# Optimization experiments

Measured on AMD Instinct MI355X. Metric: run time of the kernel, lower is better.

The kernel has to match this reference:

```python
import jax, jax.numpy as jnp
import numpy as np

ALPHA = 0.05
GDEP = 3
HID = 20  # self.hidden_num in the torch module


def setup_inputs() -> dict:
    key = jax.random.key(0)
    ks = jax.random.split(key, 6)
    B, C_IN, N, C = 8, 32, 1024, 16
    C_OUT = 32
    x = jax.random.normal(ks[0], (B, C_IN, N, C), dtype=jnp.float32)
    adj = jax.random.uniform(ks[1], (B, C, N, N), dtype=jnp.float32)
    W_start = jax.random.normal(ks[2], (C_IN, HID), dtype=jnp.float32) / np.sqrt(C_IN)
    b_start = jax.random.normal(ks[3], (HID,), dtype=jnp.float32) * 0.01
    W_end = jax.random.normal(ks[4], (HID * (GDEP + 1), C_OUT), dtype=jnp.float32) / np.sqrt(HID * (GDEP + 1))
    b_end = jax.random.normal(ks[5], (C_OUT,), dtype=jnp.float32) * 0.01
    return {"x": x, "adj": adj, "W_start": W_start, "b_start": b_start,
            "W_end": W_end, "b_end": b_end}


def reference(x, adj, W_start, b_start, W_end, b_end):
    # x: [B, c_in, N, C]; adj: [B, C, N, N]
    N = adj.shape[-1]
    # vectorized degree normalization: A_hat = (A + I) / rowsum(A + I)
    A = adj + jnp.eye(N, dtype=adj.dtype)
    A = A / A.sum(axis=-1, keepdims=True)
    # transpose(1,3) then mlp_start -> h0: [B, C, N, HID]
    xt = jnp.transpose(x, (0, 3, 2, 1))
    h0 = jnp.einsum('bcni,ih->bcnh', xt, W_start) + b_start
    h = h0
    outs = [h0]
    for _ in range(GDEP):
        # torch einsum 'ncwl,ncvw->ncvl' == A[b,c,v,w] @ h[b,c,w,l]
        h = ALPHA * h0 + (1.0 - ALPHA) * jnp.einsum('bcvw,bcwh->bcvh', A, h)
        outs.append(h)
    ho = jnp.concatenate(outs, axis=-1)  # [B, C, N, HID*(GDEP+1)]
    return jnp.einsum('bcnk,ko->bcno', ho, W_end) + b_end
```

## Files before the change

### kernel.cpp

```cpp
#include <hip/hip_runtime.h>
#include <hip/hip_bf16.h>
#include <stdint.h>

#define ALPHA 0.05f
constexpr int B_   = 8;
constexpr int CIN  = 32;
constexpr int NN   = 1024;
constexpr int CC   = 16;
constexpr int HID_ = 20;
constexpr int COUT = 32;
constexpr int PAIRS = B_ * CC;

typedef __attribute__((ext_vector_type(8))) short bf8;
typedef __attribute__((ext_vector_type(4))) float f4;

__device__ inline unsigned short f2bf(float x) {
    union { float f; uint32_t u; } v; v.f = x;
    uint32_t u = v.u;
    u += 0x7fffu + ((u >> 16) & 1u);
    return (unsigned short)(u >> 16);
}

__device__ inline bf8 pack8(float4 lo, float4 hi) {
    bf8 r;
    r[0] = (short)f2bf(lo.x); r[1] = (short)f2bf(lo.y);
    r[2] = (short)f2bf(lo.z); r[3] = (short)f2bf(lo.w);
    r[4] = (short)f2bf(hi.x); r[5] = (short)f2bf(hi.y);
    r[6] = (short)f2bf(hi.z); r[7] = (short)f2bf(hi.w);
    return r;
}

__global__ __launch_bounds__(256) void k_h0(const float* __restrict__ x,
                                            const float* __restrict__ Ws,
                                            const float* __restrict__ bs,
                                            float* __restrict__ h0) {
    int b = blockIdx.y, n0 = blockIdx.x * 16;
    __shared__ float xs[CIN * 16 * CC];
    __shared__ float WsS[CIN * HID_];
    __shared__ float bsS[HID_];
    int t = threadIdx.x;

    #pragma unroll
    for (int j = 0; j < 8; j++) {
        int idx = t + j * 256;
        int i = idx >> 6, f = idx & 63;
        ((float4*)xs)[idx] =
            ((const float4*)(x + ((size_t)(b * CIN + i) * NN + n0) * CC))[f];
    }
    for (int j = t; j < CIN * HID_; j += 256) WsS[j] = Ws[j];
    if (t < HID_) bsS[t] = bs[t];
    __syncthreads();

    int c = t & 15, nl = t >> 4;
    float acc[HID_];
    #pragma unroll
    for (int l = 0; l < HID_; l++) acc[l] = bsS[l];
    for (int i = 0; i < CIN; i++) {
        float xv = xs[i * 256 + nl * 16 + c];
        #pragma unroll
        for (int l = 0; l < HID_; l++) acc[l] += xv * WsS[i * HID_ + l];
    }
    float* dst = h0 + ((size_t)(b * CC + c) * NN + (n0 + nl)) * HID_;
    #pragma unroll
    for (int l = 0; l < HID_; l++) dst[l] = acc[l];
}

constexpr int BSTR = 1032;

__global__ __launch_bounds__(512, 4) void k_prop(
        const float* __restrict__ adj,
        const float* __restrict__ h_in,
        const float* __restrict__ h0,
        float* __restrict__ h_out) {
    int pair = blockIdx.y;
    int m0 = blockIdx.x * 256;
    __shared__ unsigned short Ht[32 * BSTR];
    int t = threadIdx.x;
    int lane = t & 63, wave = t >> 6;
    int ml = lane & 15, quad = lane >> 4;

    const float* hp = h_in + (size_t)pair * NN * HID_;
    for (int k = t; k < NN; k += 512) {
        float4 v0 = *(const float4*)(hp + (size_t)k * HID_ + 0);
        float4 v1 = *(const float4*)(hp + (size_t)k * HID_ + 4);
        float4 v2 = *(const float4*)(hp + (size_t)k * HID_ + 8);
        float4 v3 = *(const float4*)(hp + (size_t)k * HID_ + 12);
        float4 v4 = *(const float4*)(hp + (size_t)k * HID_ + 16);
        float vv[20] = {v0.x, v0.y, v0.z, v0.w, v1.x, v1.y, v1.z, v1.w,
                        v2.x, v2.y, v2.z, v2.w, v3.x, v3.y, v3.z, v3.w,
                        v4.x, v4.y, v4.z, v4.w};
        #pragma unroll
        for (int l = 0; l < HID_; l++) Ht[l * BSTR + k] = f2bf(vv[l]);
    }
    {
        uint4 ones; ones.x = ones.y = ones.z = ones.w = 0x3F803F80u;
        uint4 zero; zero.x = zero.y = zero.z = zero.w = 0u;
        for (int idx = t; idx < 12 * (NN / 8); idx += 512) {
            int row = 20 + (idx >> 7), seg = idx & 127;
            *(uint4*)&Ht[row * BSTR + seg * 8] = (row == 20) ? ones : zero;
        }
    }
    __syncthreads();

    f4 acc[2][2];
    #pragma unroll
    for (int mt = 0; mt < 2; mt++)
        #pragma unroll
        for (int nt = 0; nt < 2; nt++)
            #pragma unroll
            for (int r = 0; r < 4; r++) acc[mt][nt][r] = 0.0f;

    const float* a0p = adj + ((size_t)pair * NN + (m0 + wave * 32 + ml)) * NN + quad * 8;
    const float* a1p = a0p + (size_t)16 * NN;
    const int b0off = ml * BSTR + quad * 8;
    const int b1off = b0off + 16 * BSTR;

    float4 c00 = *(const float4*)(a0p + 0);
    float4 c01 = *(const float4*)(a0p + 4);
    float4 c10 = *(const float4*)(a1p + 0);
    float4 c11 = *(const float4*)(a1p + 4);

    #pragma unroll 1
    for (int ks = 0; ks < NN; ks += 64) {
        float4 n00 = *(const float4*)(a0p + ks + 32);
        float4 n01 = *(const float4*)(a0p + ks + 36);
        float4 n10 = *(const float4*)(a1p + ks + 32);
        float4 n11 = *(const float4*)(a1p + ks + 36);
        {
            bf8 b0 = *(const bf8*)&Ht[b0off + ks];
            bf8 b1 = *(const bf8*)&Ht[b1off + ks];
            bf8 a0 = pack8(c00, c01);
            bf8 a1 = pack8(c10, c11);
            acc[0][0] = __builtin_amdgcn_mfma_f32_16x16x32_bf16(a0, b0, acc[0][0], 0, 0, 0);
            acc[0][1] = __builtin_amdgcn_mfma_f32_16x16x32_bf16(a0, b1, acc[0][1], 0, 0, 0);
            acc[1][0] = __builtin_amdgcn_mfma_f32_16x16x32_bf16(a1, b0, acc[1][0], 0, 0, 0);
            acc[1][1] = __builtin_amdgcn_mfma_f32_16x16x32_bf16(a1, b1, acc[1][1], 0, 0, 0);
        }
        int k2 = (ks + 64 < NN) ? (ks + 64) : 0;
        c00 = *(const float4*)(a0p + k2);
        c01 = *(const float4*)(a0p + k2 + 4);
        c10 = *(const float4*)(a1p + k2);
        c11 = *(const float4*)(a1p + k2 + 4);
        {
            bf8 b0 = *(const bf8*)&Ht[b0off + ks + 32];
            bf8 b1 = *(const bf8*)&Ht[b1off + ks + 32];
            bf8 a0 = pack8(n00, n01);
            bf8 a1 = pack8(n10, n11);
            acc[0][0] = __builtin_amdgcn_mfma_f32_16x16x32_bf16(a0, b0, acc[0][0], 0, 0, 0);
            acc[0][1] = __builtin_amdgcn_mfma_f32_16x16x32_bf16(a0, b1, acc[0][1], 0, 0, 0);
            acc[1][0] = __builtin_amdgcn_mfma_f32_16x16x32_bf16(a1, b0, acc[1][0], 0, 0, 0);
            acc[1][1] = __builtin_amdgcn_mfma_f32_16x16x32_bf16(a1, b1, acc[1][1], 0, 0, 0);
        }
    }

    #pragma unroll
    for (int mt = 0; mt < 2; mt++) {
        #pragma unroll
        for (int r = 0; r < 4; r++) {
            int row = m0 + wave * 32 + mt * 16 + quad * 4 + r;
            float s = __shfl(acc[mt][1][r], (quad << 4) + 4, 64) + 1.0f;
            float inv_s = (1.0f - ALPHA) / s;
            {
                size_t off = ((size_t)pair * NN + row) * HID_ + ml;
                h_out[off] = ALPHA * h0[off] + inv_s * (acc[mt][0][r] + h_in[off]);
            }
            if (ml < 4) {
                size_t off = ((size_t)pair * NN + row) * HID_ + 16 + ml;
                h_out[off] = ALPHA * h0[off] + inv_s * (acc[mt][1][r] + h_in[off]);
            }
        }
    }
}

__global__ __launch_bounds__(256) void k_out(const float* __restrict__ h0,
                                             const float* __restrict__ h1,
                                             const float* __restrict__ h2,
                                             const float* __restrict__ h3,
                                             const float* __restrict__ We,
                                             const float* __restrict__ be,
                                             float* __restrict__ out) {
    int pair = blockIdx.y, n0 = blockIdx.x * 128;
    int t = threadIdx.x;
    __shared__ float WeT[32 * 84];
    __shared__ float beS[32];
    for (int idx = t; idx < 80 * 32; idx += 256) {
        int k = idx >> 5, o = idx & 31;
        WeT[o * 84 + k] = We[idx];
    }
    if (t < 32) beS[t] = be[t];
    __syncthreads();

    const float* hs[4] = {h0, h1, h2, h3};
    int og = t & 7, ng = t >> 3;
    float acc[4][4];
    #pragma unroll
    for (int r = 0; r < 4; r++)
        #pragma unroll
        for (int c = 0; c < 4; c++) acc[r][c] = beS[og + c * 8];

    #pragma unroll
    for (int src = 0; src < 4; src++) {
        const float* hp = hs[src] + ((size_t)pair * NN + n0 + ng) * HID_;
        #pragma unroll
        for (int j = 0; j < 5; j++) {
            float4 hv[4];
            #pragma unroll
            for (int r = 0; r < 4; r++)
                hv[r] = *(const float4*)(hp + (size_t)(r * 32) * HID_ + j * 4);
            #pragma unroll
            for (int c = 0; c < 4; c++) {
                float4 wv = *(const float4*)&WeT[(og + c * 8) * 84 + src * 20 + j * 4];
                #pragma unroll
                for (int r = 0; r < 4; r++)
                    acc[r][c] += hv[r].x * wv.x + hv[r].y * wv.y +
                                 hv[r].z * wv.z + hv[r].w * wv.w;
            }
        }
    }
    #pragma unroll
    for (int r = 0; r < 4; r++)
        #pragma unroll
        for (int c = 0; c < 4; c++)
            out[((size_t)pair * NN + n0 + ng + r * 32) * COUT + og + c * 8] = acc[r][c];
}

extern "C" void kernel_launch(void* const* d_in, const int* in_sizes, int n_in,
                              void* d_out, int out_size, void* d_ws, size_t ws_size,
                              hipStream_t stream) {
    const float* x   = (const float*)d_in[0];
    const float* adj = (const float*)d_in[1];
    const float* Ws  = (const float*)d_in[2];
    const float* bs  = (const float*)d_in[3];
    const float* We  = (const float*)d_in[4];
    const float* be  = (const float*)d_in[5];
    float* out = (float*)d_out;

    const size_t HSZ = (size_t)PAIRS * NN * HID_;
    float* h0 = (float*)d_ws;
    float* h1 = h0 + HSZ;
    float* h2 = h1 + HSZ;
    float* h3 = h2 + HSZ;

    k_h0  <<<dim3(64, 8),    256, 0, stream>>>(x, Ws, bs, h0);
    k_prop<<<dim3(4, PAIRS), 512, 0, stream>>>(adj, h0, h0, h1);
    k_prop<<<dim3(4, PAIRS), 512, 0, stream>>>(adj, h1, h0, h2);
    k_prop<<<dim3(4, PAIRS), 512, 0, stream>>>(adj, h2, h0, h3);
    k_out <<<dim3(8, PAIRS), 256, 0, stream>>>(h0, h1, h2, h3, We, be, out);
}
```

Baseline: 1.051 ms.

## Pre-convert adjacency to bf16 in MFMA-fragment layout once, reuse across propagation steps

Adds a conversion kernel that turns the fp32 adjacency into bf16, stored in a swizzled layout that matches the MFMA A-operand fragment order. The three propagation kernels then read the half-size bf16 tiles directly instead of re-reading fp32 and converting per step. This removes the repeated conversion ALU work and halves per-step adjacency bandwidth. The cost is an extra full read of fp32 and a write of the bf16 copy, plus a larger workspace requirement.

```diff
diff --git a/kernel.cpp b/kernel.cpp
--- a/kernel.cpp
+++ b/kernel.cpp
@@ -1,5 +1,4 @@
 #include <hip/hip_runtime.h>
-#include <hip/hip_bf16.h>
 #include <stdint.h>
 
 #define ALPHA 0.05f
@@ -21,13 +20,40 @@
     return (unsigned short)(u >> 16);
 }
 
-__device__ inline bf8 pack8(float4 lo, float4 hi) {
-    bf8 r;
-    r[0] = (short)f2bf(lo.x); r[1] = (short)f2bf(lo.y);
-    r[2] = (short)f2bf(lo.z); r[3] = (short)f2bf(lo.w);
-    r[4] = (short)f2bf(hi.x); r[5] = (short)f2bf(hi.y);
-    r[6] = (short)f2bf(hi.z); r[7] = (short)f2bf(hi.w);
-    return r;
+constexpr int CSTR = 268;
+
+__global__ __launch_bounds__(256) void k_conv(const float* __restrict__ adj,
+                                              unsigned short* __restrict__ Asw) {
+    int pair = blockIdx.y;
+    int rb = blockIdx.x >> 2;
+    int cb = blockIdx.x & 3;
+    __shared__ unsigned short T[64 * CSTR];
+    int t = threadIdx.x;
+
+    const float* src = adj + ((size_t)pair * NN + rb * 64) * NN + cb * 256;
+    #pragma unroll
+    for (int j = 0; j < 16; j++) {
+        int idx = j * 256 + t;
+        int row = idx >> 6, c4 = idx & 63;
+        float4 v = *(const float4*)(src + (size_t)row * NN + c4 * 4);
+        ushort4 w;
+        w.x = f2bf(v.x); w.y = f2bf(v.y); w.z = f2bf(v.z); w.w = f2bf(v.w);
+        *(ushort4*)&T[row * CSTR + c4 * 4] = w;
+    }
+    __syncthreads();
+
+    int lane = t & 63, wave = t >> 6;
+    int ml = lane & 15, quad = lane >> 4;
+    unsigned short* dst = Asw +
+        (((size_t)pair * 64 + rb * 4 + wave) * 32 + cb * 8) * 512 + lane * 8;
+    const unsigned short* srcT = &T[(wave * 16 + ml) * CSTR + quad * 8];
+    #pragma unroll
+    for (int kb = 0; kb < 8; kb++) {
+        uint2 lo = *(const uint2*)(srcT + kb * 32);
+        uint2 hi = *(const uint2*)(srcT + kb * 32 + 4);
+        uint4 o; o.x = lo.x; o.y = lo.y; o.z = hi.x; o.w = hi.y;
+        *(uint4*)(dst + (size_t)kb * 512) = o;
+    }
 }
 
 __global__ __launch_bounds__(256) void k_h0(const float* __restrict__ x,
@@ -68,7 +94,7 @@
 constexpr int BSTR = 1032;
 
 __global__ __launch_bounds__(512, 4) void k_prop(
-        const float* __restrict__ adj,
+        const unsigned short* __restrict__ Asw,
         const float* __restrict__ h_in,
         const float* __restrict__ h0,
         float* __restrict__ h_out) {
@@ -110,47 +136,42 @@
             #pragma unroll
             for (int r = 0; r < 4; r++) acc[mt][nt][r] = 0.0f;
 
-    const float* a0p = adj + ((size_t)pair * NN + (m0 + wave * 32 + ml)) * NN + quad * 8;
-    const float* a1p = a0p + (size_t)16 * NN;
+    const unsigned short* At0 = Asw +
+        ((size_t)pair * 64 + blockIdx.x * 16 + wave * 2) * (32 * 512) + lane * 8;
+    const unsigned short* At1 = At0 + 32 * 512;
     const int b0off = ml * BSTR + quad * 8;
     const int b1off = b0off + 16 * BSTR;
 
-    float4 c00 = *(const float4*)(a0p + 0);
-    float4 c01 = *(const float4*)(a0p + 4);
-    float4 c10 = *(const float4*)(a1p + 0);
-    float4 c11 = *(const float4*)(a1p + 4);
+    bf8 cA0 = *(const bf8*)(At0);
+    bf8 cA1 = *(const bf8*)(At1);
+    bf8 cB0 = *(const bf8*)(At0 + 512);
+    bf8 cB1 = *(const bf8*)(At1 + 512);
 
     #pragma unroll 1
     for (int ks = 0; ks < NN; ks += 64) {
-        float4 n00 = *(const float4*)(a0p + ks + 32);
-        float4 n01 = *(const float4*)(a0p + ks + 36);
-        float4 n10 = *(const float4*)(a1p + ks + 32);
-        float4 n11 = *(const float4*)(a1p + ks + 36);
+        int kb = ks >> 5;
+        int kn = (kb + 2 < 32) ? (kb + 2) : 0;
+        bf8 nA0 = *(const bf8*)(At0 + kn * 512);
+        bf8 nA1 = *(const bf8*)(At1 + kn * 512);
+        bf8 nB0 = *(const bf8*)(At0 + kn * 512 + 512);
+        bf8 nB1 = *(const bf8*)(At1 + kn * 512 + 512);
         {
             bf8 b0 = *(const bf8*)&Ht[b0off + ks];
             bf8 b1 = *(const bf8*)&Ht[b1off + ks];
-            bf8 a0 = pack8(c00, c01);
-            bf8 a1 = pack8(c10, c11);
-            acc[0][0] = __builtin_amdgcn_mfma_f32_16x16x32_bf16(a0, b0, acc[0][0], 0, 0, 0);
-            acc[0][1] = __builtin_amdgcn_mfma_f32_16x16x32_bf16(a0, b1, acc[0][1], 0, 0, 0);
-            acc[1][0] = __builtin_amdgcn_mfma_f32_16x16x32_bf16(a1, b0, acc[1][0], 0, 0, 0);
-            acc[1][1] = __builtin_amdgcn_mfma_f32_16x16x32_bf16(a1, b1, acc[1][1], 0, 0, 0);
-        }
-        int k2 = (ks + 64 < NN) ? (ks + 64) : 0;
-        c00 = *(const float4*)(a0p + k2);
-        c01 = *(const float4*)(a0p + k2 + 4);
-        c10 = *(const float4*)(a1p + k2);
-        c11 = *(const float4*)(a1p + k2 + 4);
+            acc[0][0] = __builtin_amdgcn_mfma_f32_16x16x32_bf16(cA0, b0, acc[0][0], 0, 0, 0);
+            acc[0][1] = __builtin_amdgcn_mfma_f32_16x16x32_bf16(cA0, b1, acc[0][1], 0, 0, 0);
+            acc[1][0] = __builtin_amdgcn_mfma_f32_16x16x32_bf16(cA1, b0, acc[1][0], 0, 0, 0);
+            acc[1][1] = __builtin_amdgcn_mfma_f32_16x16x32_bf16(cA1, b1, acc[1][1], 0, 0, 0);
+        }
         {
             bf8 b0 = *(const bf8*)&Ht[b0off + ks + 32];
             bf8 b1 = *(const bf8*)&Ht[b1off + ks + 32];
-            bf8 a0 = pack8(n00, n01);
-            bf8 a1 = pack8(n10, n11);
-            acc[0][0] = __builtin_amdgcn_mfma_f32_16x16x32_bf16(a0, b0, acc[0][0], 0, 0, 0);
-            acc[0][1] = __builtin_amdgcn_mfma_f32_16x16x32_bf16(a0, b1, acc[0][1], 0, 0, 0);
-            acc[1][0] = __builtin_amdgcn_mfma_f32_16x16x32_bf16(a1, b0, acc[1][0], 0, 0, 0);
-            acc[1][1] = __builtin_amdgcn_mfma_f32_16x16x32_bf16(a1, b1, acc[1][1], 0, 0, 0);
-        }
+            acc[0][0] = __builtin_amdgcn_mfma_f32_16x16x32_bf16(cB0, b0, acc[0][0], 0, 0, 0);
+            acc[0][1] = __builtin_amdgcn_mfma_f32_16x16x32_bf16(cB0, b1, acc[0][1], 0, 0, 0);
+            acc[1][0] = __builtin_amdgcn_mfma_f32_16x16x32_bf16(cB1, b0, acc[1][0], 0, 0, 0);
+            acc[1][1] = __builtin_amdgcn_mfma_f32_16x16x32_bf16(cB1, b1, acc[1][1], 0, 0, 0);
+        }
+        cA0 = nA0; cA1 = nA1; cB0 = nB0; cB1 = nB1;
     }
 
     #pragma unroll
@@ -240,10 +261,12 @@
     float* h1 = h0 + HSZ;
     float* h2 = h1 + HSZ;
     float* h3 = h2 + HSZ;
-
-    k_h0  <<<dim3(64, 8),    256, 0, stream>>>(x, Ws, bs, h0);
-    k_prop<<<dim3(4, PAIRS), 512, 0, stream>>>(adj, h0, h0, h1);
-    k_prop<<<dim3(4, PAIRS), 512, 0, stream>>>(adj, h1, h0, h2);
-    k_prop<<<dim3(4, PAIRS), 512, 0, stream>>>(adj, h2, h0, h3);
-    k_out <<<dim3(8, PAIRS), 256, 0, stream>>>(h0, h1, h2, h3, We, be, out);
-}
+    unsigned short* Asw = (unsigned short*)(h3 + HSZ);
+
+    k_conv<<<dim3(64, PAIRS), 256, 0, stream>>>(adj, Asw);
+    k_h0  <<<dim3(64, 8),     256, 0, stream>>>(x, Ws, bs, h0);
+    k_prop<<<dim3(4, PAIRS),  512, 0, stream>>>(Asw, h0, h0, h1);
+    k_prop<<<dim3(4, PAIRS),  512, 0, stream>>>(Asw, h1, h0, h2);
+    k_prop<<<dim3(4, PAIRS),  512, 0, stream>>>(Asw, h2, h0, h3);
+    k_out <<<dim3(8, PAIRS),  256, 0, stream>>>(h0, h1, h2, h3, We, be, out);
+}
```

New measurement: 957.6 us. -8.9%, faster.
